# Optimization experiments

Measured on AMD Instinct MI355X. Metric: run time of the kernel, lower is better.

The kernel has to match this reference:

```python
import jax, jax.numpy as jnp
import numpy as np

SIGMA = 0.01        # config['fscore_sigma']
FSCORE_W = 0.1      # config['fscore_weight']
TASK_W = 1.0        # config['task_weight']
DOMAIN_W = 0.1      # config['domain_weight']


def setup_inputs() -> dict:
    key = jax.random.key(0)
    ks = jax.random.split(key, 11)
    B, N, M, F = 8, 4096, 4096, 512
    H1, H2, D = 256, 128, 6
    return {
        "pred_pc": jax.random.normal(ks[0], (B, N, 3), jnp.float32),
        "target_pc": jax.random.normal(ks[1], (B, M, 3), jnp.float32),
        "domain_features": jax.random.normal(ks[2], (B, F), jnp.float32),
        "dataset_weights": jax.random.uniform(ks[3], (B,), jnp.float32, 0.9, 1.2),
        "W1": jax.random.normal(ks[4], (F, H1), jnp.float32) * 0.02,
        "b1": jnp.zeros((H1,), jnp.float32),
        "W2": jax.random.normal(ks[5], (H1, H2), jnp.float32) * 0.02,
        "b2": jnp.zeros((H2,), jnp.float32),
        "W3": jax.random.normal(ks[6], (H2, D), jnp.float32) * 0.02,
        "b3": jnp.zeros((D,), jnp.float32),
        "domain_labels": jax.random.randint(ks[7], (B,), 0, D),
    }


def _chamfer_mins(pred, tgt):
    # pred: [B,N,3], tgt: [B,M,3] -> squared pairwise dists [B,N,M], then dual mins
    d = (jnp.sum(pred ** 2, axis=2)[:, :, None]
         + jnp.sum(tgt ** 2, axis=2)[:, None, :]
         - 2.0 * jnp.einsum('bnd,bmd->bnm', pred, tgt))
    return jnp.min(d, axis=2), jnp.min(d, axis=1)   # [B,N], [B,M]


def reference(pred_pc, target_pc, domain_features, dataset_weights,
              W1, b1, W2, b2, W3, b3, domain_labels):
    min_a, min_b = _chamfer_mins(pred_pc, target_pc)
    c = 2.0 * SIGMA * SIGMA
    soft_a = jnp.exp(-min_a / c)
    soft_b = jnp.exp(-min_b / c)

    # batch-level task loss (compute_reconstruction_loss on full batch)
    chamfer = jnp.mean(min_a) + jnp.mean(min_b)
    prec = jnp.mean(soft_a)
    rec = jnp.mean(soft_b)
    fscore = 2.0 * prec * rec / (prec + rec + 1e-8)
    task = chamfer + FSCORE_W * (1.0 - fscore)

    # per-sample dataset-weighted loss (vectorized form of the Python loop)
    ch_i = jnp.mean(min_a, axis=1) + jnp.mean(min_b, axis=1)
    p_i = jnp.mean(soft_a, axis=1)
    r_i = jnp.mean(soft_b, axis=1)
    f_i = 2.0 * p_i * r_i / (p_i + r_i + 1e-8)
    loss_i = ch_i + FSCORE_W * (1.0 - f_i)
    dataset_weighted = jnp.mean(dataset_weights * loss_i)

    # domain loss: GRL is identity in forward; classifier in eval mode (dropout off)
    h = jax.nn.relu(domain_features @ W1 + b1)
    h = jax.nn.relu(h @ W2 + b2)
    logits = h @ W3 + b3
    logp = jax.nn.log_softmax(logits, axis=-1)
    domain = -jnp.mean(jnp.take_along_axis(logp, domain_labels[:, None], axis=1))

    total = TASK_W * task + DOMAIN_W * domain + dataset_weighted
    return total
```

## Files before the change

### kernel.cpp

```cpp
#include <hip/hip_runtime.h>
#include <math.h>

#define B 8
#define NPTS 4096
#define SPLITS 8
#define REFS 512
#define QPT 8
#define THREADS 256

__global__ __launch_bounds__(THREADS) void chamfer_kernel(
    const float* __restrict__ pred, const float* __restrict__ targ,
    float* __restrict__ partial) {
  int id = blockIdx.x;
  int split  = id & 7;
  int qchunk = (id >> 3) & 1;
  int b      = (id >> 4) & 7;
  int dir    = id >> 7;
  const float* qp = dir ? targ : pred;
  const float* rp = dir ? pred : targ;

  __shared__ float4 refs[REFS];
  int tid = threadIdx.x;
  const float* rb = rp + ((size_t)b * NPTS + (size_t)split * REFS) * 3;
  for (int i = tid; i < REFS; i += THREADS) {
    float x = rb[i * 3 + 0], y = rb[i * 3 + 1], z = rb[i * 3 + 2];
    refs[i] = make_float4(x, y, z, 0.5f * (x * x + y * y + z * z));
  }
  __syncthreads();

  const float* qb = qp + (size_t)b * NPTS * 3;
  int q0 = qchunk * (QPT * THREADS) + tid;
  float qx[QPT], qy[QPT], qz[QPT], vmin[QPT];
#pragma unroll
  for (int i = 0; i < QPT; ++i) {
    int q = q0 + i * THREADS;
    qx[i] = qb[q * 3 + 0];
    qy[i] = qb[q * 3 + 1];
    qz[i] = qb[q * 3 + 2];
    vmin[i] = 3.4e38f;
  }

#pragma unroll 2
  for (int j = 0; j < REFS; j += 2) {
    float4 ta = refs[j];
    float4 tb = refs[j + 1];
#pragma unroll
    for (int i = 0; i < QPT; ++i) {
      float sa = fmaf(-qx[i], ta.x, fmaf(-qy[i], ta.y, fmaf(-qz[i], ta.z, ta.w)));
      float sb = fmaf(-qx[i], tb.x, fmaf(-qy[i], tb.y, fmaf(-qz[i], tb.z, tb.w)));
      vmin[i] = fminf(vmin[i], fminf(sa, sb));
    }
  }

  size_t base = (((size_t)dir * B + b) * SPLITS + split) * NPTS;
#pragma unroll
  for (int i = 0; i < QPT; ++i) {
    float qn = fmaf(qx[i], qx[i], fmaf(qy[i], qy[i], qz[i] * qz[i]));
    partial[base + q0 + i * THREADS] = fmaf(2.f, vmin[i], qn);
  }
}

__global__ __launch_bounds__(THREADS) void reduce_kernel(
    const float* __restrict__ partial, float* __restrict__ sums2) {
  int id = blockIdx.x;
  int chunk = id & 7;
  int b   = (id >> 3) & 7;
  int dir = id >> 6;
  int tid = threadIdx.x;
  size_t pb = ((size_t)dir * B + b) * SPLITS * NPTS;

  float s_min = 0.f, s_soft = 0.f;
#pragma unroll
  for (int i = 0; i < 2; ++i) {
    int q = chunk * 512 + i * 256 + tid;
    float m = 3.4e38f;
#pragma unroll
    for (int s = 0; s < SPLITS; ++s)
      m = fminf(m, partial[pb + (size_t)s * NPTS + q]);
    s_min  += m;
    s_soft += __expf(-5000.0f * m);
  }
  for (int off = 32; off > 0; off >>= 1) {
    s_min  += __shfl_down(s_min,  off);
    s_soft += __shfl_down(s_soft, off);
  }
  __shared__ float red[8];
  int wave = tid >> 6, lane = tid & 63;
  if (lane == 0) { red[wave * 2] = s_min; red[wave * 2 + 1] = s_soft; }
  __syncthreads();
  if (tid == 0) {
    float a = 0.f, c = 0.f;
    for (int w = 0; w < 4; ++w) { a += red[w * 2]; c += red[w * 2 + 1]; }
    sums2[id * 2] = a;
    sums2[id * 2 + 1] = c;
  }
}

__global__ __launch_bounds__(THREADS) void l1_kernel(
    const float* __restrict__ x, const float* __restrict__ W1,
    float* __restrict__ h1p) {
  int b  = blockIdx.x >> 3;
  int kc = blockIdx.x & 7;
  int tid = threadIdx.x;
  __shared__ float xs[64];
  if (tid < 64) xs[tid] = x[b * 512 + kc * 64 + tid];
  __syncthreads();
  float acc = 0.f;
  const float* w = W1 + (size_t)(kc * 64) * 256 + tid;
#pragma unroll 8
  for (int k = 0; k < 64; ++k) acc = fmaf(xs[k], w[k * 256], acc);
  h1p[(b * 8 + kc) * 256 + tid] = acc;
}

__global__ __launch_bounds__(128) void l2_kernel(
    const float* __restrict__ h1p, const float* __restrict__ b1,
    const float* __restrict__ W2, float* __restrict__ h2p) {
  int b  = blockIdx.x >> 1;
  int kc = blockIdx.x & 1;
  int tid = threadIdx.x;
  __shared__ float hs[128];
  {
    int k = kc * 128 + tid;
    float a = b1[k];
#pragma unroll
    for (int p = 0; p < 8; ++p) a += h1p[(b * 8 + p) * 256 + k];
    hs[tid] = fmaxf(a, 0.f);
  }
  __syncthreads();
  float acc = 0.f;
  const float* w = W2 + (size_t)(kc * 128) * 128 + tid;
#pragma unroll 8
  for (int k = 0; k < 128; ++k) acc = fmaf(hs[k], w[k * 128], acc);
  h2p[(b * 2 + kc) * 128 + tid] = acc;
}

__global__ __launch_bounds__(THREADS) void final_kernel(
    const float* __restrict__ h2p, const float* __restrict__ b2,
    const float* __restrict__ W3, const float* __restrict__ b3,
    const int* __restrict__ labels, const float* __restrict__ sums2,
    const float* __restrict__ w, float* __restrict__ out) {
  int tid = threadIdx.x;
  __shared__ float h2s[8 * 128];
  __shared__ float lg[48];
  __shared__ float nlls[8];
  __shared__ float sred_min[16];
  __shared__ float sred_soft[16];

  for (int i = tid; i < 1024; i += THREADS) {
    int b = i >> 7, j = i & 127;
    float a = b2[j] + h2p[(b * 2 + 0) * 128 + j] + h2p[(b * 2 + 1) * 128 + j];
    h2s[i] = fmaxf(a, 0.f);
  }
  if (tid >= 64 && tid < 192) {
    int t = tid - 64;
    float mn = sums2[2 * t], sf = sums2[2 * t + 1];
    for (int off = 4; off > 0; off >>= 1) {
      mn += __shfl_down(mn, off, 8);
      sf += __shfl_down(sf, off, 8);
    }
    if ((t & 7) == 0) { sred_min[t >> 3] = mn; sred_soft[t >> 3] = sf; }
  }
  __syncthreads();
  if (tid < 48) {
    int b = tid / 6, d = tid % 6;
    float acc = b3[d];
#pragma unroll 8
    for (int k = 0; k < 128; ++k) acc = fmaf(h2s[b * 128 + k], W3[k * 6 + d], acc);
    lg[tid] = acc;
  }
  __syncthreads();
  if (tid < 8) {
    int b = tid;
    float mx = lg[b * 6];
    for (int d = 1; d < 6; ++d) mx = fmaxf(mx, lg[b * 6 + d]);
    float se = 0.f;
    for (int d = 0; d < 6; ++d) se += __expf(lg[b * 6 + d] - mx);
    int lab = labels[b];
    nlls[b] = -(lg[b * 6 + lab] - mx - __logf(se));
  }
  __syncthreads();
  if (tid == 0) {
    float chamfer = 0.f, prec = 0.f, rec = 0.f, dsw = 0.f, dom = 0.f;
    for (int b = 0; b < B; ++b) {
      float sa = sred_min[b],      ssa = sred_soft[b];
      float sb = sred_min[8 + b],  ssb = sred_soft[8 + b];
      float ma = sa / 4096.f, mb = sb / 4096.f;
      float p = ssa / 4096.f, r = ssb / 4096.f;
      chamfer += ma + mb;
      prec += p; rec += r;
      float f_i = 2.f * p * r / (p + r + 1e-8f);
      float loss_i = ma + mb + 0.1f * (1.f - f_i);
      dsw += w[b] * loss_i;
      dom += nlls[b];
    }
    chamfer *= (1.f / B); prec *= (1.f / B); rec *= (1.f / B);
    dsw *= (1.f / B); dom *= (1.f / B);
    float fscore = 2.f * prec * rec / (prec + rec + 1e-8f);
    float task = chamfer + 0.1f * (1.f - fscore);
    out[0] = 1.0f * task + 0.1f * dom + dsw;
  }
}

extern "C" void kernel_launch(void* const* d_in, const int* in_sizes, int n_in,
                              void* d_out, int out_size, void* d_ws, size_t ws_size,
                              hipStream_t stream) {
  const float* pred   = (const float*)d_in[0];
  const float* targ   = (const float*)d_in[1];
  const float* x      = (const float*)d_in[2];
  const float* wgt    = (const float*)d_in[3];
  const float* W1     = (const float*)d_in[4];
  const float* b1     = (const float*)d_in[5];
  const float* W2     = (const float*)d_in[6];
  const float* b2     = (const float*)d_in[7];
  const float* W3     = (const float*)d_in[8];
  const float* b3     = (const float*)d_in[9];
  const int*   labels = (const int*)d_in[10];
  float* out = (float*)d_out;

  char* ws = (char*)d_ws;
  float* partial = (float*)ws;
  float* sums2   = (float*)(ws + (size_t)2 * B * SPLITS * NPTS * sizeof(float));
  float* h1p     = sums2 + 256;
  float* h2p     = h1p + 8 * 8 * 256;

  hipLaunchKernelGGL(chamfer_kernel, dim3(256), dim3(THREADS), 0, stream,
                     pred, targ, partial);
  hipLaunchKernelGGL(reduce_kernel, dim3(128), dim3(THREADS), 0, stream,
                     partial, sums2);
  hipLaunchKernelGGL(l1_kernel, dim3(64), dim3(THREADS), 0, stream,
                     x, W1, h1p);
  hipLaunchKernelGGL(l2_kernel, dim3(16), dim3(128), 0, stream,
                     h1p, b1, W2, h2p);
  hipLaunchKernelGGL(final_kernel, dim3(1), dim3(THREADS), 0, stream,
                     h2p, b2, W3, b3, labels, sums2, wgt, out);
}
```

Before: 131.6 us.

## Fuse MLP layers into chamfer kernels, raise split count, use atomic per-batch sums

Merges the first MLP layer into the chamfer distance kernel and the second MLP layer into the reduction kernel as extra blocks, cutting the launch count from five to three. The reference set is split into up to 32 chunks depending on workspace size, giving many more blocks for better occupancy on the CU count. The inner loop is unrolled to eight references with a min tree. Reduction blocks use atomicAdd into per-batch sums instead of having the final kernel combine partials. In exchange, the partial-min buffer grows and there is more reduction traffic; atomic float order also makes results nondeterministic.

```diff
diff --git a/kernel.cpp b/kernel.cpp
--- a/kernel.cpp
+++ b/kernel.cpp
@@ -3,28 +3,48 @@
 
 #define B 8
 #define NPTS 4096
-#define SPLITS 8
-#define REFS 512
 #define QPT 8
 #define THREADS 256
 
-__global__ __launch_bounds__(THREADS) void chamfer_kernel(
+
+template<int S, int LOG2S>
+__global__ __launch_bounds__(THREADS, 4) void d1_kernel(
     const float* __restrict__ pred, const float* __restrict__ targ,
-    float* __restrict__ partial) {
+    const float* __restrict__ x, const float* __restrict__ W1,
+    float* __restrict__ partial, float* __restrict__ sums32,
+    float* __restrict__ h1p) {
+  constexpr int REFS = NPTS / S;
   int id = blockIdx.x;
-  int split  = id & 7;
-  int qchunk = (id >> 3) & 1;
-  int b      = (id >> 4) & 7;
-  int dir    = id >> 7;
+  int tid = threadIdx.x;
+
+  __shared__ float4 refs[REFS];
+  __shared__ float xs[64];
+
+  if (id < 64) {
+    if (id == 0 && tid < 32) sums32[tid] = 0.f;
+    int b = id >> 3, kc = id & 7;
+    if (tid < 64) xs[tid] = x[b * 512 + kc * 64 + tid];
+    __syncthreads();
+    float acc = 0.f;
+    const float* w = W1 + (size_t)(kc * 64) * 256 + tid;
+#pragma unroll 8
+    for (int k = 0; k < 64; ++k) acc = fmaf(xs[k], w[k * 256], acc);
+    h1p[(b * 8 + kc) * 256 + tid] = acc;
+    return;
+  }
+
+  int cid = id - 64;
+  int split  = cid & (S - 1);
+  int qchunk = (cid >> LOG2S) & 1;
+  int b      = (cid >> (LOG2S + 1)) & 7;
+  int dir    = cid >> (LOG2S + 4);
   const float* qp = dir ? targ : pred;
   const float* rp = dir ? pred : targ;
 
-  __shared__ float4 refs[REFS];
-  int tid = threadIdx.x;
   const float* rb = rp + ((size_t)b * NPTS + (size_t)split * REFS) * 3;
   for (int i = tid; i < REFS; i += THREADS) {
-    float x = rb[i * 3 + 0], y = rb[i * 3 + 1], z = rb[i * 3 + 2];
-    refs[i] = make_float4(x, y, z, 0.5f * (x * x + y * y + z * z));
+    float xx = rb[i * 3 + 0], yy = rb[i * 3 + 1], zz = rb[i * 3 + 2];
+    refs[i] = make_float4(xx, yy, zz, 0.5f * (xx * xx + yy * yy + zz * zz));
   }
   __syncthreads();
 
@@ -40,19 +60,25 @@
     vmin[i] = 3.4e38f;
   }
 
-#pragma unroll 2
-  for (int j = 0; j < REFS; j += 2) {
-    float4 ta = refs[j];
-    float4 tb = refs[j + 1];
+  for (int j = 0; j < REFS; j += 8) {
+    float4 t[8];
+#pragma unroll
+    for (int u = 0; u < 8; ++u) t[u] = refs[j + u];
 #pragma unroll
     for (int i = 0; i < QPT; ++i) {
-      float sa = fmaf(-qx[i], ta.x, fmaf(-qy[i], ta.y, fmaf(-qz[i], ta.z, ta.w)));
-      float sb = fmaf(-qx[i], tb.x, fmaf(-qy[i], tb.y, fmaf(-qz[i], tb.z, tb.w)));
-      vmin[i] = fminf(vmin[i], fminf(sa, sb));
-    }
-  }
-
-  size_t base = (((size_t)dir * B + b) * SPLITS + split) * NPTS;
+      float s[8];
+#pragma unroll
+      for (int u = 0; u < 8; ++u)
+        s[u] = fmaf(-qx[i], t[u].x,
+               fmaf(-qy[i], t[u].y, fmaf(-qz[i], t[u].z, t[u].w)));
+      float m01 = fminf(s[0], s[1]), m23 = fminf(s[2], s[3]);
+      float m45 = fminf(s[4], s[5]), m67 = fminf(s[6], s[7]);
+      vmin[i] = fminf(vmin[i],
+                      fminf(fminf(m01, m23), fminf(m45, m67)));
+    }
+  }
+
+  size_t base = (((size_t)dir * B + b) * S + split) * NPTS;
 #pragma unroll
   for (int i = 0; i < QPT; ++i) {
     float qn = fmaf(qx[i], qx[i], fmaf(qy[i], qy[i], qz[i] * qz[i]));
@@ -60,26 +86,49 @@
   }
 }
 
-__global__ __launch_bounds__(THREADS) void reduce_kernel(
-    const float* __restrict__ partial, float* __restrict__ sums2) {
+template<int S>
+__global__ __launch_bounds__(THREADS) void d2_kernel(
+    const float* __restrict__ partial, float* __restrict__ sums32,
+    const float* __restrict__ h1p, const float* __restrict__ b1,
+    const float* __restrict__ W2, float* __restrict__ h2p) {
   int id = blockIdx.x;
-  int chunk = id & 7;
-  int b   = (id >> 3) & 7;
-  int dir = id >> 6;
   int tid = threadIdx.x;
-  size_t pb = ((size_t)dir * B + b) * SPLITS * NPTS;
-
-  float s_min = 0.f, s_soft = 0.f;
-#pragma unroll
-  for (int i = 0; i < 2; ++i) {
-    int q = chunk * 512 + i * 256 + tid;
-    float m = 3.4e38f;
-#pragma unroll
-    for (int s = 0; s < SPLITS; ++s)
-      m = fminf(m, partial[pb + (size_t)s * NPTS + q]);
-    s_min  += m;
-    s_soft += __expf(-5000.0f * m);
-  }
+
+  if (id >= 256) {
+    int lid = id - 256;
+    int b = lid >> 1, half = lid & 1;
+    __shared__ float hs[128];
+    if (tid < 128) {
+      int k = half * 128 + tid;
+      float a = b1[k];
+#pragma unroll
+      for (int p = 0; p < 8; ++p) a += h1p[(b * 8 + p) * 256 + k];
+      hs[tid] = fmaxf(a, 0.f);
+    }
+    __syncthreads();
+    if (tid < 128) {
+      float acc = 0.f;
+      const float* w = W2 + (size_t)(half * 128) * 128 + tid;
+#pragma unroll 8
+      for (int k = 0; k < 128; ++k) acc = fmaf(hs[k], w[k * 128], acc);
+      h2p[(b * 2 + half) * 128 + tid] = acc;
+    }
+    return;
+  }
+
+  int chunk = id & 15;
+  int b   = (id >> 4) & 7;
+  int dir = id >> 7;
+  size_t pb = ((size_t)dir * B + b) * S * NPTS;
+  int q = chunk * 256 + tid;
+
+  float m = 3.4e38f;
+#pragma unroll
+  for (int s = 0; s < S; ++s)
+    m = fminf(m, partial[pb + (size_t)s * NPTS + q]);
+  float s_min = m;
+  float s_soft = __expf(-5000.0f * m);
+
   for (int off = 32; off > 0; off >>= 1) {
     s_min  += __shfl_down(s_min,  off);
     s_soft += __shfl_down(s_soft, off);
@@ -91,74 +140,25 @@
   if (tid == 0) {
     float a = 0.f, c = 0.f;
     for (int w = 0; w < 4; ++w) { a += red[w * 2]; c += red[w * 2 + 1]; }
-    sums2[id * 2] = a;
-    sums2[id * 2 + 1] = c;
-  }
-}
-
-__global__ __launch_bounds__(THREADS) void l1_kernel(
-    const float* __restrict__ x, const float* __restrict__ W1,
-    float* __restrict__ h1p) {
-  int b  = blockIdx.x >> 3;
-  int kc = blockIdx.x & 7;
-  int tid = threadIdx.x;
-  __shared__ float xs[64];
-  if (tid < 64) xs[tid] = x[b * 512 + kc * 64 + tid];
-  __syncthreads();
-  float acc = 0.f;
-  const float* w = W1 + (size_t)(kc * 64) * 256 + tid;
-#pragma unroll 8
-  for (int k = 0; k < 64; ++k) acc = fmaf(xs[k], w[k * 256], acc);
-  h1p[(b * 8 + kc) * 256 + tid] = acc;
-}
-
-__global__ __launch_bounds__(128) void l2_kernel(
-    const float* __restrict__ h1p, const float* __restrict__ b1,
-    const float* __restrict__ W2, float* __restrict__ h2p) {
-  int b  = blockIdx.x >> 1;
-  int kc = blockIdx.x & 1;
-  int tid = threadIdx.x;
-  __shared__ float hs[128];
-  {
-    int k = kc * 128 + tid;
-    float a = b1[k];
-#pragma unroll
-    for (int p = 0; p < 8; ++p) a += h1p[(b * 8 + p) * 256 + k];
-    hs[tid] = fmaxf(a, 0.f);
-  }
-  __syncthreads();
-  float acc = 0.f;
-  const float* w = W2 + (size_t)(kc * 128) * 128 + tid;
-#pragma unroll 8
-  for (int k = 0; k < 128; ++k) acc = fmaf(hs[k], w[k * 128], acc);
-  h2p[(b * 2 + kc) * 128 + tid] = acc;
+    atomicAdd(&sums32[(dir * B + b) * 2 + 0], a);
+    atomicAdd(&sums32[(dir * B + b) * 2 + 1], c);
+  }
 }
 
 __global__ __launch_bounds__(THREADS) void final_kernel(
     const float* __restrict__ h2p, const float* __restrict__ b2,
     const float* __restrict__ W3, const float* __restrict__ b3,
-    const int* __restrict__ labels, const float* __restrict__ sums2,
+    const int* __restrict__ labels, const float* __restrict__ sums32,
     const float* __restrict__ w, float* __restrict__ out) {
   int tid = threadIdx.x;
   __shared__ float h2s[8 * 128];
   __shared__ float lg[48];
   __shared__ float nlls[8];
-  __shared__ float sred_min[16];
-  __shared__ float sred_soft[16];
 
   for (int i = tid; i < 1024; i += THREADS) {
     int b = i >> 7, j = i & 127;
     float a = b2[j] + h2p[(b * 2 + 0) * 128 + j] + h2p[(b * 2 + 1) * 128 + j];
     h2s[i] = fmaxf(a, 0.f);
-  }
-  if (tid >= 64 && tid < 192) {
-    int t = tid - 64;
-    float mn = sums2[2 * t], sf = sums2[2 * t + 1];
-    for (int off = 4; off > 0; off >>= 1) {
-      mn += __shfl_down(mn, off, 8);
-      sf += __shfl_down(sf, off, 8);
-    }
-    if ((t & 7) == 0) { sred_min[t >> 3] = mn; sred_soft[t >> 3] = sf; }
   }
   __syncthreads();
   if (tid < 48) {
@@ -182,8 +182,10 @@
   if (tid == 0) {
     float chamfer = 0.f, prec = 0.f, rec = 0.f, dsw = 0.f, dom = 0.f;
     for (int b = 0; b < B; ++b) {
-      float sa = sred_min[b],      ssa = sred_soft[b];
-      float sb = sred_min[8 + b],  ssb = sred_soft[8 + b];
+      float sa  = sums32[(0 * B + b) * 2 + 0];
+      float ssa = sums32[(0 * B + b) * 2 + 1];
+      float sb  = sums32[(1 * B + b) * 2 + 0];
+      float ssb = sums32[(1 * B + b) * 2 + 1];
       float ma = sa / 4096.f, mb = sb / 4096.f;
       float p = ssa / 4096.f, r = ssb / 4096.f;
       chamfer += ma + mb;
@@ -199,6 +201,25 @@
     float task = chamfer + 0.1f * (1.f - fscore);
     out[0] = 1.0f * task + 0.1f * dom + dsw;
   }
+}
+
+template<int S, int LOG2S>
+static void run_pipeline(const float* pred, const float* targ, const float* x,
+                         const float* wgt, const float* W1, const float* b1,
+                         const float* W2, const float* b2, const float* W3,
+                         const float* b3, const int* labels, float* out,
+                         char* ws, hipStream_t stream) {
+  float* partial = (float*)ws;
+  float* sums32  = partial + (size_t)2 * B * S * NPTS;
+  float* h1p     = sums32 + 32;
+  float* h2p     = h1p + 64 * 256;
+
+  hipLaunchKernelGGL((d1_kernel<S, LOG2S>), dim3(64 + 32 * S), dim3(THREADS),
+                     0, stream, pred, targ, x, W1, partial, sums32, h1p);
+  hipLaunchKernelGGL((d2_kernel<S>), dim3(256 + 16), dim3(THREADS), 0, stream,
+                     partial, sums32, h1p, b1, W2, h2p);
+  hipLaunchKernelGGL(final_kernel, dim3(1), dim3(THREADS), 0, stream,
+                     h2p, b2, W3, b3, labels, sums32, wgt, out);
 }
 
 extern "C" void kernel_launch(void* const* d_in, const int* in_sizes, int n_in,
@@ -216,21 +237,18 @@
   const float* b3     = (const float*)d_in[9];
   const int*   labels = (const int*)d_in[10];
   float* out = (float*)d_out;
-
   char* ws = (char*)d_ws;
-  float* partial = (float*)ws;
-  float* sums2   = (float*)(ws + (size_t)2 * B * SPLITS * NPTS * sizeof(float));
-  float* h1p     = sums2 + 256;
-  float* h2p     = h1p + 8 * 8 * 256;
-
-  hipLaunchKernelGGL(chamfer_kernel, dim3(256), dim3(THREADS), 0, stream,
-                     pred, targ, partial);
-  hipLaunchKernelGGL(reduce_kernel, dim3(128), dim3(THREADS), 0, stream,
-                     partial, sums2);
-  hipLaunchKernelGGL(l1_kernel, dim3(64), dim3(THREADS), 0, stream,
-                     x, W1, h1p);
-  hipLaunchKernelGGL(l2_kernel, dim3(16), dim3(128), 0, stream,
-                     h1p, b1, W2, h2p);
-  hipLaunchKernelGGL(final_kernel, dim3(1), dim3(THREADS), 0, stream,
-                     h2p, b2, W3, b3, labels, sums2, wgt, out);
-}
+
+  auto need = [](int S) {
+    return ((size_t)2 * B * S * NPTS + 32 + 64 * 256 + 16 * 128) * sizeof(float);
+  };
+  if (ws_size >= need(32))
+    run_pipeline<32, 5>(pred, targ, x, wgt, W1, b1, W2, b2, W3, b3, labels,
+                        out, ws, stream);
+  else if (ws_size >= need(16))
+    run_pipeline<16, 4>(pred, targ, x, wgt, W1, b1, W2, b2, W3, b3, labels,
+                        out, ws, stream);
+  else
+    run_pipeline<8, 3>(pred, targ, x, wgt, W1, b1, W2, b2, W3, b3, labels,
+                       out, ws, stream);
+}
```

Result: faster. 112.6 us (-14.5%).
